# Optimization experiments

Measured on AMD Instinct MI355X. Metric: run time of the kernel, lower is better.

The kernel has to match this reference:

```python
import jax, jax.numpy as jnp
import numpy as np

DIM = 512
HEADS = 8
EPS = 1e-5


def layer_norm(x, g, b):
    mu = jnp.mean(x, axis=-1, keepdims=True)
    var = jnp.mean(jnp.square(x - mu), axis=-1, keepdims=True)
    return (x - mu) * jax.lax.rsqrt(var + EPS) * g + b


def setup_inputs() -> dict:
    key = jax.random.key(0)
    ks = jax.random.split(key, 8)
    d = DIM
    s = 0.02
    return {
        "x": jax.random.normal(ks[0], (2, d, 64, 64), jnp.float32),
        "ln1_g": jnp.ones((d,), jnp.float32),
        "ln1_b": jnp.zeros((d,), jnp.float32),
        "w_qkv": jax.random.normal(ks[1], (d, 3 * d), jnp.float32) * s,
        "b_qkv": jnp.zeros((3 * d,), jnp.float32),
        "w_proj": jax.random.normal(ks[2], (d, d), jnp.float32) * s,
        "b_proj": jnp.zeros((d,), jnp.float32),
        "ln2_g": jnp.ones((d,), jnp.float32),
        "ln2_b": jnp.zeros((d,), jnp.float32),
        "w_ffn1": jax.random.normal(ks[3], (d, 4 * d), jnp.float32) * s,
        "b_ffn1": jnp.zeros((4 * d,), jnp.float32),
        "w_ffn2": jax.random.normal(ks[4], (4 * d, d), jnp.float32) * s,
        "b_ffn2": jnp.zeros((d,), jnp.float32),
    }


def reference(x, ln1_g, ln1_b, w_qkv, b_qkv, w_proj, b_proj,
              ln2_g, ln2_b, w_ffn1, b_ffn1, w_ffn2, b_ffn2):
    B, C, H, W = x.shape
    hd = C // HEADS
    x_in = x
    t = x.reshape(B, C, H * W).transpose(0, 2, 1)  # [B, N, C]
    h = layer_norm(t, ln1_g, ln1_b)
    qkv = h @ w_qkv + b_qkv  # [B, N, 3C]
    q, k, v = jnp.split(qkv, 3, axis=-1)
    def to_heads(a):
        return a.reshape(B, -1, HEADS, hd).transpose(0, 2, 1, 3)  # [B, h, N, hd]
    q, k, v = to_heads(q), to_heads(k), to_heads(v)
    # NOTE: module scales by 1/sqrt(C), not 1/sqrt(head_dim)
    attn = jnp.einsum('bhqd,bhkd->bhqk', q, k) / jnp.sqrt(jnp.float32(C))
    attn = jax.nn.softmax(attn, axis=-1)
    out = jnp.einsum('bhqk,bhkd->bhqd', attn, v)
    out = out.transpose(0, 2, 1, 3).reshape(B, -1, C)
    out = out @ w_proj + b_proj
    t = t + out
    h2 = layer_norm(t, ln2_g, ln2_b)
    ffn = jax.nn.relu(h2 @ w_ffn1 + b_ffn1) @ w_ffn2 + b_ffn2
    t = t + ffn
    y = t.transpose(0, 2, 1).reshape(B, C, H, W)
    return y + x_in
```

## Files before the change

### kernel.cpp

```cpp
#include <hip/hip_runtime.h>
#include <hip/hip_bf16.h>

typedef __bf16 bf16;
typedef __bf16 bf16x8 __attribute__((ext_vector_type(8)));
typedef __bf16 bf16x4 __attribute__((ext_vector_type(4)));
typedef __bf16 bf16x2 __attribute__((ext_vector_type(2)));
typedef float f32x4 __attribute__((ext_vector_type(4)));
typedef int int4v __attribute__((ext_vector_type(4)));
typedef int int2v __attribute__((ext_vector_type(2)));

#define DEV static __device__ __forceinline__

DEV void gload16(const void* g, void* l) {
    __builtin_amdgcn_global_load_lds(
        (const __attribute__((address_space(1))) void*)g,
        (__attribute__((address_space(3))) void*)l, 16, 0, 0);
}

DEV f32x4 mfma16(bf16x8 a, bf16x8 b, f32x4 c) {
    return __builtin_amdgcn_mfma_f32_16x16x32_bf16(a, b, c, 0, 0, 0);
}

DEV int cvtpk(float lo, float hi) {
    int r;
    asm("v_cvt_pk_bf16_f32 %0, %1, %2" : "=v"(r) : "v"(lo), "v"(hi));
    return r;
}

DEV float rexp2(float x) {
    float r;
    asm("v_exp_f32 %0, %1" : "=v"(r) : "v"(x));
    return r;
}

template <bool HASPO>
__global__ __launch_bounds__(512)
void k_tln(const float* __restrict__ x, const bf16* __restrict__ po,
           const float* __restrict__ gg, const float* __restrict__ bb,
           bf16* __restrict__ h) {
    __shared__ bf16 big[32][520];
    __shared__ float tile[32][33];
    int bid = blockIdx.x;
    int nt = bid & 127, b = bid >> 7;
    int n0 = nt * 32;
    int tid = threadIdx.x;
    const float* xb = x + (size_t)b * 512 * 4096 + n0;
    int nl = tid & 31, cl = tid >> 5;
    int cl2 = tid & 31, nh = tid >> 5;
    for (int ct = 0; ct < 16; ct++) {
        int c0 = ct * 32;
#pragma unroll
        for (int i = 0; i < 2; i++) {
            int c = cl + i * 16;
            tile[c][nl] = xb[(size_t)(c0 + c) * 4096 + nl];
        }
        __syncthreads();
#pragma unroll
        for (int i = 0; i < 2; i++) {
            int n = nh + i * 16;
            big[n][c0 + cl2] = (bf16)tile[cl2][n];
        }
        __syncthreads();
    }
    int w = tid >> 6, l = tid & 63;
    f32x4 g0 = *(const f32x4*)(gg + l * 8);
    f32x4 g1 = *(const f32x4*)(gg + l * 8 + 4);
    f32x4 bb0 = *(const f32x4*)(bb + l * 8);
    f32x4 bb1 = *(const f32x4*)(bb + l * 8 + 4);
#pragma unroll
    for (int r = 0; r < 4; r++) {
        int n = w * 4 + r;
        bf16x8 vv = *(const bf16x8*)&big[n][l * 8];
        float v[8];
#pragma unroll
        for (int j = 0; j < 8; j++) v[j] = (float)vv[j];
        if (HASPO) {
            bf16x8 pv = *(const bf16x8*)(po +
                (size_t)(b * 4096 + n0 + n) * 512 + l * 8);
#pragma unroll
            for (int j = 0; j < 8; j++) v[j] += (float)pv[j];
        }
        float s = (((v[0] + v[1]) + (v[2] + v[3])) +
                   ((v[4] + v[5]) + (v[6] + v[7])));
#pragma unroll
        for (int m = 1; m < 64; m <<= 1) s += __shfl_xor(s, m);
        float mu = s * (1.0f / 512.0f);
        float vs = 0.f;
#pragma unroll
        for (int j = 0; j < 8; j++) {
            float d = v[j] - mu;
            vs += d * d;
        }
#pragma unroll
        for (int m = 1; m < 64; m <<= 1) vs += __shfl_xor(vs, m);
        float rs = rsqrtf(vs * (1.0f / 512.0f) + 1e-5f);
        bf16x8 o;
#pragma unroll
        for (int j = 0; j < 4; j++) {
            o[j] = (bf16)((v[j] - mu) * rs * g0[j] + bb0[j]);
            o[j + 4] = (bf16)((v[j + 4] - mu) * rs * g1[j] + bb1[j]);
        }
        *(bf16x8*)(h + (size_t)(b * 4096 + n0 + n) * 512 + l * 8) = o;
    }
}

__global__ __launch_bounds__(256)
void k_fin(const float* __restrict__ x, const bf16* __restrict__ po,
           const bf16* __restrict__ f2o, float* __restrict__ y) {
    __shared__ float ts[64][33];
    int bid = blockIdx.x;
    int nt = bid & 127, ct = (bid >> 7) & 7, b = bid >> 10;
    int n0 = nt * 32, c0 = ct * 64;
    int tid = threadIdx.x;
    int pi = tid & 31, nr = tid >> 5;
#pragma unroll
    for (int p = 0; p < 4; p++) {
        int n = nr + p * 8;
        size_t ro = (size_t)(b * 4096 + n0 + n) * 512 + c0 + pi * 2;
        bf16x2 pv = *(const bf16x2*)(po + ro);
        bf16x2 fv = *(const bf16x2*)(f2o + ro);
        ts[pi * 2][n] = (float)pv[0] + (float)fv[0];
        ts[pi * 2 + 1][n] = (float)pv[1] + (float)fv[1];
    }
    __syncthreads();
    int nw = tid & 31, cw = tid >> 5;
#pragma unroll
    for (int q = 0; q < 8; q++) {
        int c = cw + q * 8;
        size_t off = ((size_t)b * 512 + c0 + c) * 4096 + n0 + nw;
        y[off] = 2.0f * x[off] + ts[c][nw];
    }
}

__global__ __launch_bounds__(256)
void k_wtall(const float* __restrict__ w0, const float* __restrict__ w1,
             const float* __restrict__ w2, const float* __restrict__ w3,
             bf16* __restrict__ d0, bf16* __restrict__ d1,
             bf16* __restrict__ d2, bf16* __restrict__ d3) {
    __shared__ float tile[32][33];
    int bid = blockIdx.x;
    const float* w;
    bf16* d;
    int K, N, t;
    if (bid < 768)       { w = w0; d = d0; K = 512;  N = 1536; t = bid; }
    else if (bid < 1024) { w = w1; d = d1; K = 512;  N = 512;  t = bid - 768; }
    else if (bid < 2048) { w = w2; d = d2; K = 512;  N = 2048; t = bid - 1024; }
    else                 { w = w3; d = d3; K = 2048; N = 512;  t = bid - 2048; }
    int ntn = N >> 5;
    int kt = t / ntn, ntile = t % ntn;
    int k0 = kt * 32, n0 = ntile * 32;
    int tid = threadIdx.x;
    int nl = tid & 31, kl = tid >> 5;
#pragma unroll
    for (int i = 0; i < 4; i++) {
        int k = kl + i * 8;
        tile[k][nl] = w[(size_t)(k0 + k) * N + n0 + nl];
    }
    __syncthreads();
    int kl2 = tid & 31, nl2 = tid >> 5;
#pragma unroll
    for (int i = 0; i < 4; i++) {
        int n = nl2 + i * 8;
        d[(size_t)(n0 + n) * K + k0 + kl2] = (bf16)tile[kl2][n];
    }
}

template <int MODE, int BN>
__global__ __launch_bounds__(256, BN == 64 ? 3 : 2)
void k_gemm(const bf16* __restrict__ A, const bf16* __restrict__ BT,
            const float* __restrict__ bias, bf16* __restrict__ outb,
            bf16* __restrict__ vtout, int M, int N, int K) {
    constexpr int CG = BN / 32;
    constexpr int BSZ = CG * 4096;
    __shared__ char smem[32768 + 2 * BSZ];
    int ntn = N / BN;
    int nwg = gridDim.x;
    int bid = blockIdx.x;
    int cpx = nwg >> 3;
    bid = (bid & 7) * cpx + (bid >> 3);
    int bm = bid / ntn, bn = bid % ntn;
    int m0 = bm * 128, n0 = bn * BN;
    int tid = threadIdx.x;
    int w = tid >> 6, l = tid & 63;
    int wm = w >> 1, wn = w & 1;
    int l15 = l & 15, lg = l >> 4;

    f32x4 acc[4][CG];
#pragma unroll
    for (int i = 0; i < 4; i++)
#pragma unroll
        for (int j = 0; j < CG; j++) acc[i][j] = (f32x4){0.f, 0.f, 0.f, 0.f};

    int srow = tid >> 3, sphys = tid & 7;
    int lrow_a = wm * 64 + l15;
    int lrow_b = wn * (BN / 2) + l15;

#define GEMM_STAGE(k0v, bb)                                                  \
    do {                                                                     \
        _Pragma("unroll") for (int s = 0; s < 4; s++) {                      \
            int row = s * 32 + srow;                                         \
            int k16 = sphys ^ (row & 7);                                     \
            gload16(A + (size_t)(m0 + row) * K + (k0v) + k16 * 8,            \
                    smem + (bb) * 16384 + s * 4096 + tid * 16);              \
        }                                                                    \
        _Pragma("unroll") for (int s = 0; s < CG; s++) {                     \
            int row = s * 32 + srow;                                         \
            int k16 = sphys ^ (row & 7);                                     \
            gload16(BT + (size_t)(n0 + row) * K + (k0v) + k16 * 8,           \
                    smem + 32768 + (bb) * BSZ + s * 4096 + tid * 16);        \
        }                                                                    \
    } while (0)

    int nk = K >> 6;
    GEMM_STAGE(0, 0);
    int cur = 0;
    for (int kt = 0; kt < nk; kt++) {
        if (kt + 1 < nk) {
            GEMM_STAGE((kt + 1) << 6, cur ^ 1);
            if constexpr (BN == 128)
                asm volatile("s_waitcnt vmcnt(8)" ::: "memory");
            else
                asm volatile("s_waitcnt vmcnt(6)" ::: "memory");
        } else {
            asm volatile("s_waitcnt vmcnt(0)" ::: "memory");
        }
        __builtin_amdgcn_s_barrier();
        __builtin_amdgcn_sched_barrier(0);
        const char* pA = smem + cur * 16384;
        const char* pB = smem + 32768 + cur * BSZ;
#pragma unroll
        for (int ks = 0; ks < 2; ks++) {
            bf16x8 af[4], bfr[CG];
#pragma unroll
            for (int rg = 0; rg < 4; rg++) {
                int row = lrow_a + rg * 16;
                af[rg] = *(const bf16x8*)(pA + row * 128 +
                                          (((lg + ks * 4) ^ (row & 7)) << 4));
            }
#pragma unroll
            for (int cg = 0; cg < CG; cg++) {
                int row = lrow_b + cg * 16;
                bfr[cg] = *(const bf16x8*)(pB + row * 128 +
                                           (((lg + ks * 4) ^ (row & 7)) << 4));
            }
#pragma unroll
            for (int rg = 0; rg < 4; rg++)
#pragma unroll
                for (int cg = 0; cg < CG; cg++)
                    acc[rg][cg] = mfma16(af[rg], bfr[cg], acc[rg][cg]);
        }
        __builtin_amdgcn_s_barrier();
        cur ^= 1;
    }
#undef GEMM_STAGE

    if constexpr (MODE == 2) {
        if (n0 >= 1024) {
            char* vl = smem;
#pragma unroll
            for (int cg = 0; cg < CG; cg++) {
                int col = wn * 64 + cg * 16 + l15;
                float bz = bias[n0 + col];
#pragma unroll
                for (int rg = 0; rg < 4; rg++) {
                    int rowb = wm * 64 + rg * 16 + lg * 4;
                    int2v qq = {cvtpk(acc[rg][cg][0] + bz, acc[rg][cg][1] + bz),
                                cvtpk(acc[rg][cg][2] + bz, acc[rg][cg][3] + bz)};
                    *(int2v*)(vl + col * 272 + rowb * 2) = qq;
                }
            }
            __syncthreads();
            int b = m0 >> 12, nrow0 = m0 & 4095;
            int dl = tid >> 3, c8 = tid & 7;
#pragma unroll
            for (int dd = 0; dd < 4; dd++) {
                int d = dd * 32 + dl;
                int ch = (n0 - 1024) + d;
                bf16* dst = vtout +
                    ((size_t)((b * 8 + (ch >> 6)) * 64 + (ch & 63))) * 4096 + nrow0;
#pragma unroll
                for (int half = 0; half < 2; half++) {
                    int chunk = half * 8 + c8;
                    bf16x8 vv = *(const bf16x8*)(vl + d * 272 + chunk * 16);
                    *(bf16x8*)(dst + chunk * 8) = vv;
                }
            }
            return;
        }
    }

    constexpr int RS = BN * 2 + 8;
    constexpr int CH = BN / 8;
    char* ep = smem;
#pragma unroll
    for (int cg = 0; cg < CG; cg++) {
        int lcol = wn * (BN / 2) + cg * 16 + l15;
        float bz = bias[n0 + lcol];
#pragma unroll
        for (int rg = 0; rg < 4; rg++) {
#pragma unroll
            for (int j = 0; j < 4; j++) {
                int lrow = wm * 64 + rg * 16 + lg * 4 + j;
                float v = acc[rg][cg][j] + bz;
                if (MODE == 1) v = fmaxf(v, 0.f);
                *(bf16*)(ep + lrow * RS + lcol * 2) = (bf16)v;
            }
        }
    }
    __syncthreads();
    int cch = tid & (CH - 1);
    int rof = tid / CH;
    constexpr int RPP = 256 / CH;
#pragma unroll
    for (int i = 0; i < 128 / RPP; i++) {
        int row = i * RPP + rof;
        bf16x8 vv = *(const bf16x8*)(ep + row * RS + cch * 16);
        *(bf16x8*)(outb + (size_t)(m0 + row) * N + n0 + cch * 8) = vv;
    }
}

__global__ __launch_bounds__(256, 4)
void k_attn(const bf16* __restrict__ qkvb, const bf16* __restrict__ vt,
            bf16* __restrict__ attno) {
    __shared__ bf16 sK[2][64 * 64];
    __shared__ bf16 sV[2][64 * 64];
    const float sc = 0.044194173824159216f * 1.4426950408889634f;
    int bid = blockIdx.x;
    int nb = (bid & 7) * 128 + (bid >> 3);
    int bh = nb >> 6, qt = nb & 63;
    int b = bh >> 3, hh = bh & 7;
    int q0 = qt * 64;
    int tid = threadIdx.x, w = tid >> 6, l = tid & 63;
    int l15 = l & 15, lg = l >> 4, l7 = l15 & 7;
    int lg4 = lg * 4;
    int vperm = ((lg & 1) << 1) | (lg >> 1);
    const bf16* qbase = qkvb + (size_t)b * 4096 * 1536 + hh * 64;
    const bf16* kbase = qbase + 512;
    const bf16* vbase = vt + (size_t)bh * 64 * 4096;
    int srow = tid >> 3, sphys = tid & 7;

    const char* kp0 = (const char*)&sK[0][0] + l15 * 128 + ((lg ^ l7) << 4);
    const char* kp1 = (const char*)&sK[0][0] + l15 * 128 + (((4 + lg) ^ l7) << 4);
    const char* vp0 = (const char*)&sV[0][0] + l15 * 128 + ((vperm ^ l7) << 4);
    const char* vp1 = (const char*)&sV[0][0] + l15 * 128 + (((4 + vperm) ^ l7) << 4);
    char* dK0 = (char*)&sK[0][0] + tid * 16;
    char* dV0 = (char*)&sV[0][0] + tid * 16;
    const char* kg = (const char*)(kbase + srow * 1536 + (sphys ^ (srow & 7)) * 8);
    const char* vg = (const char*)(vbase + srow * 4096 + (sphys ^ (srow & 7)) * 8);

    gload16(kg, dK0);
    gload16(kg + 98304, dK0 + 4096);
    gload16(vg, dV0);
    gload16(vg + 262144, dV0 + 4096);
    kg += 196608;
    vg += 128;

    bf16x8 qf[2];
#pragma unroll
    for (int ks = 0; ks < 2; ks++) {
        bf16x8 v = *(const bf16x8*)(qbase +
            (size_t)(q0 + w * 16 + l15) * 1536 + ks * 32 + lg * 8);
        bf16x8 o;
#pragma unroll
        for (int j = 0; j < 8; j++) o[j] = (bf16)((float)v[j] * sc);
        qf[ks] = o;
    }

    const f32x4 kZ = {0.f, 0.f, 0.f, 0.f};
    float lsum = 0.f;
    f32x4 acc[4];
#pragma unroll
    for (int df = 0; df < 4; df++) acc[df] = kZ;

#define ABODY(BUF, PF)                                                        \
    {                                                                         \
        if (PF) {                                                             \
            gload16(kg, dK0 + (1 - (BUF)) * 8192);                            \
            gload16(kg + 98304, dK0 + (1 - (BUF)) * 8192 + 4096);             \
            gload16(vg, dV0 + (1 - (BUF)) * 8192);                            \
            gload16(vg + 262144, dV0 + (1 - (BUF)) * 8192 + 4096);            \
            kg += 196608;                                                     \
            vg += 128;                                                        \
            asm volatile("s_waitcnt vmcnt(4)" ::: "memory");                  \
        } else {                                                              \
            asm volatile("s_waitcnt vmcnt(0)" ::: "memory");                  \
        }                                                                     \
        __builtin_amdgcn_s_barrier();                                         \
        __builtin_amdgcn_sched_barrier(0);                                    \
        f32x4 s0, s1, s2, s3;                                                 \
        __builtin_amdgcn_s_setprio(1);                                        \
        s0 = mfma16(*(const bf16x8*)(kp0 + (BUF) * 8192 + 0 * 2048), qf[0], kZ); \
        s0 = mfma16(*(const bf16x8*)(kp1 + (BUF) * 8192 + 0 * 2048), qf[1], s0); \
        s1 = mfma16(*(const bf16x8*)(kp0 + (BUF) * 8192 + 1 * 2048), qf[0], kZ); \
        s1 = mfma16(*(const bf16x8*)(kp1 + (BUF) * 8192 + 1 * 2048), qf[1], s1); \
        __builtin_amdgcn_s_setprio(0);                                        \
        float e0 = rexp2(s0[0]), e1 = rexp2(s0[1]);                           \
        float e2 = rexp2(s0[2]), e3 = rexp2(s0[3]);                           \
        float e4 = rexp2(s1[0]), e5 = rexp2(s1[1]);                           \
        float e6 = rexp2(s1[2]), e7 = rexp2(s1[3]);                           \
        __builtin_amdgcn_s_setprio(1);                                        \
        s2 = mfma16(*(const bf16x8*)(kp0 + (BUF) * 8192 + 2 * 2048), qf[0], kZ); \
        s2 = mfma16(*(const bf16x8*)(kp1 + (BUF) * 8192 + 2 * 2048), qf[1], s2); \
        s3 = mfma16(*(const bf16x8*)(kp0 + (BUF) * 8192 + 3 * 2048), qf[0], kZ); \
        s3 = mfma16(*(const bf16x8*)(kp1 + (BUF) * 8192 + 3 * 2048), qf[1], s3); \
        __builtin_amdgcn_s_setprio(0);                                        \
        int p0 = cvtpk(e0, e1), p1 = cvtpk(e2, e3);                           \
        int p2 = cvtpk(e4, e5), p3 = cvtpk(e6, e7);                           \
        asm("v_permlane16_swap_b32 %0, %1" : "+v"(p2), "+v"(p0));             \
        asm("v_permlane16_swap_b32 %0, %1" : "+v"(p3), "+v"(p1));             \
        {                                                                     \
            int4v ai = {p0, p1, p2, p3};                                      \
            bf16x8 af = __builtin_bit_cast(bf16x8, ai);                       \
            __builtin_amdgcn_s_setprio(1);                                    \
            acc[0] = mfma16(af, *(const bf16x8*)(vp0 + (BUF) * 8192 + 0 * 2048), acc[0]); \
            acc[1] = mfma16(af, *(const bf16x8*)(vp0 + (BUF) * 8192 + 1 * 2048), acc[1]); \
            acc[2] = mfma16(af, *(const bf16x8*)(vp0 + (BUF) * 8192 + 2 * 2048), acc[2]); \
            acc[3] = mfma16(af, *(const bf16x8*)(vp0 + (BUF) * 8192 + 3 * 2048), acc[3]); \
            __builtin_amdgcn_s_setprio(0);                                    \
        }                                                                     \
        float e8 = rexp2(s2[0]), e9 = rexp2(s2[1]);                           \
        float e10 = rexp2(s2[2]), e11 = rexp2(s2[3]);                         \
        float e12 = rexp2(s3[0]), e13 = rexp2(s3[1]);                         \
        float e14 = rexp2(s3[2]), e15 = rexp2(s3[3]);                         \
        int p4 = cvtpk(e8, e9), p5 = cvtpk(e10, e11);                         \
        int p6 = cvtpk(e12, e13), p7 = cvtpk(e14, e15);                       \
        asm("v_permlane16_swap_b32 %0, %1" : "+v"(p6), "+v"(p4));             \
        asm("v_permlane16_swap_b32 %0, %1" : "+v"(p7), "+v"(p5));             \
        {                                                                     \
            int4v ai = {p4, p5, p6, p7};                                      \
            bf16x8 af = __builtin_bit_cast(bf16x8, ai);                       \
            __builtin_amdgcn_s_setprio(1);                                    \
            acc[0] = mfma16(af, *(const bf16x8*)(vp1 + (BUF) * 8192 + 0 * 2048), acc[0]); \
            acc[1] = mfma16(af, *(const bf16x8*)(vp1 + (BUF) * 8192 + 1 * 2048), acc[1]); \
            acc[2] = mfma16(af, *(const bf16x8*)(vp1 + (BUF) * 8192 + 2 * 2048), acc[2]); \
            acc[3] = mfma16(af, *(const bf16x8*)(vp1 + (BUF) * 8192 + 3 * 2048), acc[3]); \
            __builtin_amdgcn_s_setprio(0);                                    \
        }                                                                     \
        lsum += (((e0 + e1) + (e2 + e3)) + ((e4 + e5) + (e6 + e7))) +         \
                (((e8 + e9) + (e10 + e11)) + ((e12 + e13) + (e14 + e15)));    \
        __builtin_amdgcn_s_barrier();                                         \
    }

    for (int tt = 0; tt < 31; tt++) {
        ABODY(0, 1)
        ABODY(1, 1)
    }
    ABODY(0, 1)
    ABODY(1, 0)
#undef ABODY

    lsum += __shfl_xor(lsum, 16);
    lsum += __shfl_xor(lsum, 32);
    float invq[4];
#pragma unroll
    for (int j = 0; j < 4; j++)
        invq[j] = 1.0f / __shfl(lsum, lg4 + j);

    bf16* ow = (bf16*)&sK[0][0] + w * 16 * 64;
#pragma unroll
    for (int df = 0; df < 4; df++) {
        int chunk = df * 2 + (l15 >> 3);
        int within = l15 & 7;
#pragma unroll
        for (int j = 0; j < 4; j++) {
            int q = lg * 4 + j;
            *(bf16*)((char*)ow + q * 128 + ((chunk ^ (q & 7)) << 4) + within * 2) =
                (bf16)(acc[df][j] * invq[j]);
        }
    }
    __syncthreads();
    const char* owr = (const char*)ow;
#pragma unroll
    for (int half = 0; half < 2; half++) {
        int r = l >> 2, ch = (l & 3) + half * 4;
        bf16x8 vv = *(const bf16x8*)(owr + r * 128 + ((ch ^ (r & 7)) << 4));
        *(bf16x8*)(attno + (size_t)(b * 4096 + q0 + w * 16 + r) * 512 +
                   hh * 64 + ch * 8) = vv;
    }
}

extern "C" void kernel_launch(void* const* d_in, const int* in_sizes, int n_in,
                              void* d_out, int out_size, void* d_ws, size_t ws_size,
                              hipStream_t stream) {
    const float* x = (const float*)d_in[0];
    const float* ln1g = (const float*)d_in[1];
    const float* ln1b = (const float*)d_in[2];
    const float* wqkv = (const float*)d_in[3];
    const float* bqkv = (const float*)d_in[4];
    const float* wproj = (const float*)d_in[5];
    const float* bproj = (const float*)d_in[6];
    const float* ln2g = (const float*)d_in[7];
    const float* ln2b = (const float*)d_in[8];
    const float* wffn1 = (const float*)d_in[9];
    const float* bffn1 = (const float*)d_in[10];
    const float* wffn2 = (const float*)d_in[11];
    const float* bffn2 = (const float*)d_in[12];
    float* y = (float*)d_out;

    char* ws = (char*)d_ws;
    bf16* po   = (bf16*)(ws + 0);
    bf16* f2o  = (bf16*)(ws + 8388608);
    bf16* h    = (bf16*)(ws + 16777216);
    bf16* qkvb = (bf16*)(ws + 25165824);
    bf16* vtb  = (bf16*)(ws + 50331648);
    bf16* f1   = (bf16*)(ws + 25165824);
    bf16* wqT  = (bf16*)(ws + 58720256);
    bf16* wpT  = (bf16*)(ws + 60293120);
    bf16* w1T  = (bf16*)(ws + 60817408);
    bf16* w2T  = (bf16*)(ws + 62914560);
    bf16* attno = h;

    k_tln<false><<<256, 512, 0, stream>>>(x, nullptr, ln1g, ln1b, h);
    k_wtall<<<3072, 256, 0, stream>>>(wqkv, wproj, wffn1, wffn2,
                                      wqT, wpT, w1T, w2T);
    k_gemm<2, 128><<<768, 256, 0, stream>>>(h, wqT, bqkv, qkvb, vtb,
                                            8192, 1536, 512);
    k_attn<<<1024, 256, 0, stream>>>(qkvb, vtb, attno);
    k_gemm<0, 64><<<512, 256, 0, stream>>>(attno, wpT, bproj, po, nullptr,
                                           8192, 512, 512);
    k_tln<true><<<256, 512, 0, stream>>>(x, po, ln2g, ln2b, h);
    k_gemm<1, 128><<<1024, 256, 0, stream>>>(h, w1T, bffn1, f1, nullptr,
                                             8192, 2048, 512);
    k_gemm<0, 64><<<512, 256, 0, stream>>>(f1, w2T, bffn2, f2o, nullptr,
                                           8192, 512, 2048);
    k_fin<<<2048, 256, 0, stream>>>(x, po, f2o, y);
}
```

Measured before the change: 204.0 us.

## Restructure transpose-layernorm kernel into a single-pass fused transpose with block reduction

Replaces the 16-iteration tiled transpose (two barriers per iteration) with a single pass. Each thread reads 32 channels for one token, accumulates sum and sum of squares, and writes bf16 values into shared memory. Mean and variance then come from a cross-wave shared-memory reduction, and the residual input is staged into LDS with vectorized loads. This cuts barriers and the separate shuffle reductions, but the one-pass variance formula is less numerically robust. It also generalizes the V-transpose epilogue in the GEMM to the BN template parameter.

```diff
diff --git a/kernel.cpp b/kernel.cpp
--- a/kernel.cpp
+++ b/kernel.cpp
@@ -34,73 +34,83 @@
 }
 
 template <bool HASPO>
-__global__ __launch_bounds__(512)
+__global__ __launch_bounds__(512, 2)
 void k_tln(const float* __restrict__ x, const bf16* __restrict__ po,
            const float* __restrict__ gg, const float* __restrict__ bb,
            bf16* __restrict__ h) {
-    __shared__ bf16 big[32][520];
-    __shared__ float tile[32][33];
+    __shared__ char sm[HASPO ? 69632 : 35840];
+    bf16* big = (bf16*)sm;
+    float* red = (float*)(sm + 33536);
+    float* mures = (float*)(sm + 35584);
+    bf16* pob = (bf16*)(sm + 35840);
+
+    int t = threadIdx.x;
     int bid = blockIdx.x;
     int nt = bid & 127, b = bid >> 7;
     int n0 = nt * 32;
-    int tid = threadIdx.x;
-    const float* xb = x + (size_t)b * 512 * 4096 + n0;
-    int nl = tid & 31, cl = tid >> 5;
-    int cl2 = tid & 31, nh = tid >> 5;
-    for (int ct = 0; ct < 16; ct++) {
-        int c0 = ct * 32;
-#pragma unroll
-        for (int i = 0; i < 2; i++) {
-            int c = cl + i * 16;
-            tile[c][nl] = xb[(size_t)(c0 + c) * 4096 + nl];
-        }
+
+    if (HASPO) {
+        int rr = t >> 4, cs16 = t & 15;
+        const bf16* ps = po + (size_t)(b * 4096 + n0 + rr) * 512 + cs16 * 32;
+#pragma unroll
+        for (int j = 0; j < 4; j++)
+            *(bf16x8*)&pob[rr * 524 + cs16 * 32 + j * 8] =
+                *(const bf16x8*)(ps + j * 8);
         __syncthreads();
-#pragma unroll
-        for (int i = 0; i < 2; i++) {
-            int n = nh + i * 16;
-            big[n][c0 + cl2] = (bf16)tile[cl2][n];
-        }
-        __syncthreads();
-    }
-    int w = tid >> 6, l = tid & 63;
-    f32x4 g0 = *(const f32x4*)(gg + l * 8);
-    f32x4 g1 = *(const f32x4*)(gg + l * 8 + 4);
-    f32x4 bb0 = *(const f32x4*)(bb + l * 8);
-    f32x4 bb1 = *(const f32x4*)(bb + l * 8 + 4);
-#pragma unroll
-    for (int r = 0; r < 4; r++) {
-        int n = w * 4 + r;
-        bf16x8 vv = *(const bf16x8*)&big[n][l * 8];
-        float v[8];
-#pragma unroll
-        for (int j = 0; j < 8; j++) v[j] = (float)vv[j];
-        if (HASPO) {
-            bf16x8 pv = *(const bf16x8*)(po +
-                (size_t)(b * 4096 + n0 + n) * 512 + l * 8);
-#pragma unroll
-            for (int j = 0; j < 8; j++) v[j] += (float)pv[j];
-        }
-        float s = (((v[0] + v[1]) + (v[2] + v[3])) +
-                   ((v[4] + v[5]) + (v[6] + v[7])));
-#pragma unroll
-        for (int m = 1; m < 64; m <<= 1) s += __shfl_xor(s, m);
-        float mu = s * (1.0f / 512.0f);
-        float vs = 0.f;
-#pragma unroll
-        for (int j = 0; j < 8; j++) {
-            float d = v[j] - mu;
-            vs += d * d;
-        }
-#pragma unroll
-        for (int m = 1; m < 64; m <<= 1) vs += __shfl_xor(vs, m);
-        float rs = rsqrtf(vs * (1.0f / 512.0f) + 1e-5f);
+    }
+
+    int n = t & 31, cg = t >> 5;
+    const float* xp = x + (size_t)b * 512 * 4096 +
+                      (size_t)(cg * 32) * 4096 + n0 + n;
+    float s = 0.f, ss = 0.f;
+#pragma unroll
+    for (int i = 0; i < 32; i++) {
+        float v = xp[(size_t)i * 4096];
+        if (HASPO) v += (float)pob[n * 524 + cg * 32 + i];
+        s += v;
+        ss += v * v;
+        big[n * 524 + cg * 32 + i] = (bf16)v;
+    }
+    s += __shfl_xor(s, 32);
+    ss += __shfl_xor(ss, 32);
+    int w = t >> 6, l = t & 63;
+    if (l < 32) {
+        red[(w * 32 + n) * 2] = s;
+        red[(w * 32 + n) * 2 + 1] = ss;
+    }
+    __syncthreads();
+    if (t < 32) {
+        float ts = 0.f, tss = 0.f;
+#pragma unroll
+        for (int ww = 0; ww < 8; ww++) {
+            ts += red[(ww * 32 + t) * 2];
+            tss += red[(ww * 32 + t) * 2 + 1];
+        }
+        float mu = ts * (1.f / 512.f);
+        float var = tss * (1.f / 512.f) - mu * mu;
+        mures[t * 2] = mu;
+        mures[t * 2 + 1] = rsqrtf(var + 1e-5f);
+    }
+    __syncthreads();
+
+    int nw = t >> 4, cs = t & 15;
+    float mu = mures[nw * 2], rs = mures[nw * 2 + 1];
+    bf16* hd = h + (size_t)(b * 4096 + n0 + nw) * 512;
+#pragma unroll
+    for (int j = 0; j < 4; j++) {
+        int c = cs * 8 + j * 128;
+        bf16x8 vv = *(const bf16x8*)&big[nw * 524 + c];
+        f32x4 g0v = *(const f32x4*)(gg + c);
+        f32x4 g1v = *(const f32x4*)(gg + c + 4);
+        f32x4 b0v = *(const f32x4*)(bb + c);
+        f32x4 b1v = *(const f32x4*)(bb + c + 4);
         bf16x8 o;
 #pragma unroll
-        for (int j = 0; j < 4; j++) {
-            o[j] = (bf16)((v[j] - mu) * rs * g0[j] + bb0[j]);
-            o[j + 4] = (bf16)((v[j + 4] - mu) * rs * g1[j] + bb1[j]);
-        }
-        *(bf16x8*)(h + (size_t)(b * 4096 + n0 + n) * 512 + l * 8) = o;
+        for (int k = 0; k < 4; k++) {
+            o[k] = (bf16)(((float)vv[k] - mu) * rs * g0v[k] + b0v[k]);
+            o[k + 4] = (bf16)(((float)vv[k + 4] - mu) * rs * g1v[k] + b1v[k]);
+        }
+        *(bf16x8*)(hd + c) = o;
     }
 }
 
@@ -259,7 +269,7 @@
             char* vl = smem;
 #pragma unroll
             for (int cg = 0; cg < CG; cg++) {
-                int col = wn * 64 + cg * 16 + l15;
+                int col = wn * (BN / 2) + cg * 16 + l15;
                 float bz = bias[n0 + col];
 #pragma unroll
                 for (int rg = 0; rg < 4; rg++) {
@@ -273,7 +283,7 @@
             int b = m0 >> 12, nrow0 = m0 & 4095;
             int dl = tid >> 3, c8 = tid & 7;
 #pragma unroll
-            for (int dd = 0; dd < 4; dd++) {
+            for (int dd = 0; dd < BN / 32; dd++) {
                 int d = dd * 32 + dl;
                 int ch = (n0 - 1024) + d;
                 bf16* dst = vtout +
```

Result: faster. 188.6 us (-7.5%).
